# Kernel optimization log

Hardware: AMD Instinct MI355X
Metric: run time of the kernel (lower is better)

The kernel has to match this reference:

```python
import jax, jax.numpy as jnp
import numpy as np


def setup_inputs() -> dict:
    key = jax.random.key(0)
    k1, k2, k3 = jax.random.split(key, 3)
    N, C, V, T, K = 32, 64, 25, 1024, 3
    x = jax.random.normal(k1, (N, C, V, T), dtype=jnp.float32)
    # grouped 1x1 conv weight: per node v, maps C -> K*C. torch weight (C*K*V, C, 1, 1)
    W = jax.random.normal(k2, (V, K * C, C), dtype=jnp.float32) * 0.05
    # adjacency buffer A[k, w, v] (src node w -> dst node v, partition k)
    A = jax.random.uniform(k3, (K, V, V), dtype=jnp.float32)
    return {"x": x, "W": W, "A": A}


def reference(x, W, A):
    # x: [N, C, V, T]; W: [V, K*C, C]; A: [K, V, V]
    N, C, V, T = x.shape
    K = A.shape[0]
    # permute(0,2,1,3): [N, V, C, T]; grouped 1x1 conv == per-node matmul C -> K*C
    y = jnp.einsum('ncvt,voc->nvot', x, W)          # [N, V, K*C, T]
    # view (N, V, C*K, T) with output-channel layout o = c*K + k -> split to (C, K)
    y = y.reshape(N, V, C, K, T)                     # [N, V(src=w), C, K, T]
    # einsum('kwv,nckwt->ncvt')
    out = jnp.einsum('kwv,nwckt->ncvt', A, y)        # [N, C, V, T]
    return out
```

## Files before the change

### kernel.cpp

```cpp
#include <hip/hip_runtime.h>

#define Nn 32
#define Cc 64
#define Vv 25
#define Tt 1024

typedef __attribute__((ext_vector_type(4))) float f32x4;
typedef __attribute__((ext_vector_type(8))) short bf16x8;
typedef __attribute__((ext_vector_type(4))) unsigned short u16x4;

__device__ __forceinline__ unsigned short f2bf(float f) {
    union { float f; unsigned u; } a; a.f = f;
    unsigned u = a.u;
    u += 0x7fff + ((u >> 16) & 1);
    return (unsigned short)(u >> 16);
}

__device__ __forceinline__ void gl_lds16(const unsigned short* g, unsigned short* l) {
    __builtin_amdgcn_global_load_lds(
        (const __attribute__((address_space(1))) unsigned int*)g,
        (__attribute__((address_space(3))) unsigned int*)l, 16, 0, 0);
}


__global__ __launch_bounds__(256) void prep_fused(
        const float* __restrict__ x, const float* __restrict__ W,
        const float* __restrict__ A, unsigned short* __restrict__ xb,
        unsigned short* __restrict__ Weff) {
    int bid = blockIdx.x;
    if (bid < Vv * Vv) {
        int v = bid / Vv;
        int w = bid - v * Vv;
        float a0 = A[(0 * Vv + w) * Vv + v];
        float a1 = A[(1 * Vv + w) * Vv + v];
        float a2 = A[(2 * Vv + w) * Vv + v];
        const float* Wb = W + (size_t)w * 192 * 64;
        unsigned short* o = Weff + (size_t)(v * Vv + w) * 4096;
        int c  = threadIdx.x >> 2;
        int c0 = (threadIdx.x & 3) * 16;
        #pragma unroll
        for (int i = 0; i < 16; ++i) {
            int cp = c0 + i;
            float val = a0 * Wb[(c * 3 + 0) * 64 + cp]
                      + a1 * Wb[(c * 3 + 1) * 64 + cp]
                      + a2 * Wb[(c * 3 + 2) * 64 + cp];
            int jl = cp >> 3;
            o[c * 64 + ((jl ^ (c & 7)) << 3) + (cp & 7)] = f2bf(val);
        }
        return;
    }
    int pid = bid - Vv * Vv;
    int n = pid / (Vv * 8);
    int rem = pid - n * (Vv * 8);
    int w = rem >> 3;
    int t0 = (rem & 7) << 7;

    int tid = threadIdx.x;
    int wv = tid >> 6;
    int l  = tid & 63;
    int jl = l & 7;
    int tg = l >> 3;

    int tbase = t0 + wv * 32 + tg * 4;
    const float* xn = x + ((size_t)(n * Cc) * Vv + w) * Tt + tbase;
    unsigned short* dst = xb + ((size_t)(n * Vv + w) * Tt) * 64;

    f32x4 f[8];
    #pragma unroll
    for (int k = 0; k < 8; ++k) {
        int r = jl * 8 + k;
        f[k] = __builtin_nontemporal_load(
            (const f32x4*)(xn + (size_t)r * (Vv * Tt)));
    }
    #pragma unroll
    for (int j = 0; j < 4; ++j) {
        bf16x8 o;
        #pragma unroll
        for (int k = 0; k < 8; ++k) o[k] = (short)f2bf(f[k][j]);
        int tl = tbase + j;
        int pc = jl ^ (tl & 7);
        *(bf16x8*)&dst[(size_t)tl * 64 + pc * 8] = o;
    }
}

__global__ __launch_bounds__(256, 2) void gc_fast(
        const unsigned short* __restrict__ xb,
        const unsigned short* __restrict__ Weff,
        float* __restrict__ out) {
    __shared__ __align__(16) unsigned short wa[8][4096];

    int bid = blockIdx.x;
    int xcd = bid & 7;
    int lid = bid >> 3;
    int v = lid % Vv;
    int s = lid / Vv;
    int slice = (xcd << 4) + s;
    int n  = slice >> 2;
    int t0 = (slice & 3) << 8;

    int tid = threadIdx.x;
    int lane = tid & 63, wv = tid >> 6;
    int m = lane & 15, quad = lane >> 4;

    const unsigned short* wg = Weff + (size_t)v * (Vv * 4096);
    const unsigned short* xbase = xb + ((size_t)(n * Vv) * Tt + t0) * 64;

    int coff0 = ((quad)     ^ (m & 7)) << 3;
    int coff1 = ((4 + quad) ^ (m & 7)) << 3;
    int trow[4], arow[4];
    #pragma unroll
    for (int ni = 0; ni < 4; ++ni) trow[ni] = (wv * 64 + ni * 16 + m) * 64;
    #pragma unroll
    for (int mi = 0; mi < 4; ++mi) arow[mi] = (mi * 16 + m) * 64;

    f32x4 acc[4][4];
    #pragma unroll
    for (int i = 0; i < 4; ++i)
        #pragma unroll
        for (int j = 0; j < 4; ++j)
            acc[i][j] = (f32x4){0.f, 0.f, 0.f, 0.f};

    bf16x8 b0v[8], b1v[8], b2v[8];

#define SB __builtin_amdgcn_sched_barrier(0)
#define VMCNT(N_) asm volatile("s_waitcnt vmcnt(" #N_ ")" ::: "memory")

#define ISSUE_A(WBUF, w_) do { \
    const unsigned short* s_ = wg + (size_t)(w_) * 4096 + tid * 8; \
    gl_lds16(s_,        &wa[WBUF][tid * 8]); \
    gl_lds16(s_ + 2048, &wa[WBUF][2048 + tid * 8]); \
} while (0)

#define ISSUE_B(BN, w_) do { \
    const unsigned short* xw_ = xbase + (size_t)(w_) * (Tt * 64); \
    _Pragma("unroll") \
    for (int ni_ = 0; ni_ < 4; ++ni_) { \
        BN[ni_]     = *(const bf16x8*)(xw_ + trow[ni_] + coff0); \
        BN[ni_ + 4] = *(const bf16x8*)(xw_ + trow[ni_] + coff1); \
    } \
} while (0)

#define COMP(RBUF, BC) do { \
    const unsigned short* cur_ = &wa[RBUF][0]; \
    bf16x8 af_[8]; \
    _Pragma("unroll") \
    for (int mi_ = 0; mi_ < 4; ++mi_) { \
        af_[mi_]     = *(const bf16x8*)(cur_ + arow[mi_] + coff0); \
        af_[mi_ + 4] = *(const bf16x8*)(cur_ + arow[mi_] + coff1); \
    } \
    __builtin_amdgcn_s_setprio(1); \
    _Pragma("unroll") \
    for (int mi_ = 0; mi_ < 4; ++mi_) \
        _Pragma("unroll") \
        for (int ni_ = 0; ni_ < 4; ++ni_) \
            acc[mi_][ni_] = __builtin_amdgcn_mfma_f32_16x16x32_bf16( \
                af_[mi_], BC[ni_], acc[mi_][ni_], 0, 0, 0); \
    _Pragma("unroll") \
    for (int mi_ = 0; mi_ < 4; ++mi_) \
        _Pragma("unroll") \
        for (int ni_ = 0; ni_ < 4; ++ni_) \
            acc[mi_][ni_] = __builtin_amdgcn_mfma_f32_16x16x32_bf16( \
                af_[mi_ + 4], BC[ni_ + 4], acc[mi_][ni_], 0, 0, 0); \
    __builtin_amdgcn_s_setprio(0); \
} while (0)

#define DSTEP(R0, R1, W4, W5, C0, C1, I2, I3, w_, N3, N6) do { \
    ISSUE_B(I2, (w_) + 2); \
    ISSUE_A(W4, (w_) + 4); \
    ISSUE_A(W5, (w_) + 5); \
    SB; VMCNT(N3); SB; \
    __builtin_amdgcn_s_barrier(); \
    SB; \
    COMP(R0, C0); \
    SB; \
    ISSUE_B(I3, (w_) + 3); \
    SB; VMCNT(N6); SB; \
    COMP(R1, C1); \
    SB; \
} while (0)

    ISSUE_B(b0v, 0);
    ISSUE_B(b1v, 1);
    ISSUE_A(0, 0);
    ISSUE_A(1, 1);
    ISSUE_A(2, 2);
    ISSUE_A(3, 3);
    SB;

    DSTEP(0, 1, 4, 5, b0v, b1v, b2v, b0v,  0, 16, 20);
    DSTEP(2, 3, 6, 7, b2v, b0v, b1v, b2v,  2, 24, 20);
    DSTEP(4, 5, 0, 1, b1v, b2v, b0v, b1v,  4, 24, 20);
    DSTEP(6, 7, 2, 3, b0v, b1v, b2v, b0v,  6, 24, 20);
    DSTEP(0, 1, 4, 5, b2v, b0v, b1v, b2v,  8, 24, 20);
    DSTEP(2, 3, 6, 7, b1v, b2v, b0v, b1v, 10, 24, 20);
    DSTEP(4, 5, 0, 1, b0v, b1v, b2v, b0v, 12, 24, 20);
    DSTEP(6, 7, 2, 3, b2v, b0v, b1v, b2v, 14, 24, 20);
    DSTEP(0, 1, 4, 5, b1v, b2v, b0v, b1v, 16, 24, 20);
    DSTEP(2, 3, 6, 7, b0v, b1v, b2v, b0v, 18, 24, 20);

    ISSUE_B(b1v, 22);
    ISSUE_A(0, 24);
    SB; VMCNT(22); SB;
    __builtin_amdgcn_s_barrier();
    SB;
    COMP(4, b2v);
    SB;
    ISSUE_B(b2v, 23);
    SB; VMCNT(18); SB;
    COMP(5, b0v);
    SB;

    ISSUE_B(b0v, 24);
    SB; VMCNT(18); SB;
    __builtin_amdgcn_s_barrier();
    SB;
    COMP(6, b1v);
    SB; VMCNT(10); SB;
    COMP(7, b2v);
    SB;

    VMCNT(0);
    SB;
    __builtin_amdgcn_s_barrier();
    SB;
    COMP(0, b0v);

#undef DSTEP
#undef COMP
#undef ISSUE_B
#undef ISSUE_A
#undef VMCNT
#undef SB

    float* og = out + ((size_t)n * Cc * Vv + v) * Tt + t0 + wv * 64 + m;
    #pragma unroll
    for (int mi = 0; mi < 4; ++mi)
        #pragma unroll
        for (int r = 0; r < 4; ++r) {
            int c = mi * 16 + quad * 4 + r;
            float* orow = og + (size_t)c * Vv * Tt;
            #pragma unroll
            for (int ni = 0; ni < 4; ++ni)
                __builtin_nontemporal_store(acc[mi][ni][r], &orow[ni * 16]);
        }
}


__global__ __launch_bounds__(256) void weff_prep_plain(
        const float* __restrict__ W, const float* __restrict__ A,
        unsigned short* __restrict__ Weff) {
    int v = blockIdx.x / Vv;
    int w = blockIdx.x - v * Vv;
    float a0 = A[(0 * Vv + w) * Vv + v];
    float a1 = A[(1 * Vv + w) * Vv + v];
    float a2 = A[(2 * Vv + w) * Vv + v];
    const float* Wb = W + (size_t)w * 192 * 64;
    unsigned short* o = Weff + (size_t)(v * Vv + w) * 4096;
    int e0 = threadIdx.x * 16;
    #pragma unroll
    for (int i = 0; i < 16; ++i) {
        int e = e0 + i;
        int c = e >> 6, cp = e & 63;
        float val = a0 * Wb[(c * 3 + 0) * 64 + cp]
                  + a1 * Wb[(c * 3 + 1) * 64 + cp]
                  + a2 * Wb[(c * 3 + 2) * 64 + cp];
        o[e] = f2bf(val);
    }
}

__global__ __launch_bounds__(256, 2) void gc_plain(
        const float* __restrict__ x, const unsigned short* __restrict__ Weff,
        float* __restrict__ out) {
    __shared__ __align__(16) unsigned short xs[256 * 72];
    __shared__ __align__(16) unsigned short wa[64 * 72];
    int bid = blockIdx.x;
    int xcd = bid & 7;
    int lid = bid >> 3;
    int v, s;
    if (lid < 13 * 16) { v = lid % 13;            s = lid / 13; }
    else { int l2 = lid - 13 * 16; v = 13 + l2 % 12; s = l2 / 12; }
    int slice = (xcd << 4) + s;
    int n  = slice >> 2;
    int t0 = (slice & 3) << 8;
    int tid  = threadIdx.x;
    int lane = tid & 63;
    int wv   = tid >> 6;
    int m    = lane & 15;
    int quad = lane >> 4;
    int cc = tid & 7;
    int tt = tid >> 3;
    f32x4 acc[4][4];
    #pragma unroll
    for (int i = 0; i < 4; ++i)
        #pragma unroll
        for (int j = 0; j < 4; ++j)
            acc[i][j] = (f32x4){0.f, 0.f, 0.f, 0.f};
    const float* xg = x + (size_t)n * Cc * Vv * Tt + t0 + tt * 4;
    const bf16x8* wg = (const bf16x8*)(Weff + (size_t)v * Vv * 4096);
    for (int w = 0; w < Vv; ++w) {
        if (w) __syncthreads();
        #pragma unroll
        for (int r = 0; r < 2; ++r) {
            int q = r * 256 + tid;
            int c = q >> 3, b = q & 7;
            *(bf16x8*)&wa[c * 72 + b * 8] = wg[w * 512 + q];
        }
        {
            bf16x8 rows[8];
            #pragma unroll
            for (int i = 0; i < 8; ++i) {
                int cp = cc * 8 + i;
                const float* p = xg + ((size_t)cp * Vv + w) * Tt;
                float4 f0 = *(const float4*)p;
                float4 f1 = *(const float4*)(p + 128);
                rows[0][i] = (short)f2bf(f0.x); rows[1][i] = (short)f2bf(f0.y);
                rows[2][i] = (short)f2bf(f0.z); rows[3][i] = (short)f2bf(f0.w);
                rows[4][i] = (short)f2bf(f1.x); rows[5][i] = (short)f2bf(f1.y);
                rows[6][i] = (short)f2bf(f1.z); rows[7][i] = (short)f2bf(f1.w);
            }
            #pragma unroll
            for (int j = 0; j < 4; ++j) {
                *(bf16x8*)&xs[(tt * 4 + j) * 72 + cc * 8]       = rows[j];
                *(bf16x8*)&xs[(128 + tt * 4 + j) * 72 + cc * 8] = rows[4 + j];
            }
        }
        __syncthreads();
        #pragma unroll
        for (int kc = 0; kc < 2; ++kc) {
            int ko = kc * 32 + quad * 8;
            bf16x8 afr[4], bfr[4];
            #pragma unroll
            for (int mi = 0; mi < 4; ++mi)
                afr[mi] = *(const bf16x8*)&wa[(mi * 16 + m) * 72 + ko];
            #pragma unroll
            for (int ni = 0; ni < 4; ++ni)
                bfr[ni] = *(const bf16x8*)&xs[(wv * 64 + ni * 16 + m) * 72 + ko];
            #pragma unroll
            for (int mi = 0; mi < 4; ++mi)
                #pragma unroll
                for (int ni = 0; ni < 4; ++ni)
                    acc[mi][ni] = __builtin_amdgcn_mfma_f32_16x16x32_bf16(
                        afr[mi], bfr[ni], acc[mi][ni], 0, 0, 0);
        }
    }
    float* og = out + ((size_t)n * Cc * Vv + v) * Tt + t0 + wv * 64 + m;
    #pragma unroll
    for (int mi = 0; mi < 4; ++mi)
        #pragma unroll
        for (int r = 0; r < 4; ++r) {
            int c = mi * 16 + quad * 4 + r;
            float* orow = og + (size_t)c * Vv * Tt;
            #pragma unroll
            for (int ni = 0; ni < 4; ++ni)
                orow[ni * 16] = acc[mi][ni][r];
        }
}

extern "C" void kernel_launch(void* const* d_in, const int* in_sizes, int n_in,
                              void* d_out, int out_size, void* d_ws, size_t ws_size,
                              hipStream_t stream) {
    const float* x = (const float*)d_in[0];
    const float* W = (const float*)d_in[1];
    const float* A = (const float*)d_in[2];
    float* out = (float*)d_out;

    const size_t xb_elems   = (size_t)Nn * Vv * Tt * 64;
    const size_t weff_elems = (size_t)Vv * Vv * 4096;
    const size_t need = (xb_elems + weff_elems) * sizeof(unsigned short);

    if (ws_size >= need) {
        unsigned short* xb   = (unsigned short*)d_ws;
        unsigned short* Weff = xb + xb_elems;
        prep_fused<<<dim3(Vv * Vv + Nn * Vv * 8), dim3(256), 0, stream>>>(x, W, A, xb, Weff);
        gc_fast<<<dim3(3200), dim3(256), 0, stream>>>(xb, Weff, out);
    } else {
        unsigned short* Weff = (unsigned short*)d_ws;
        weff_prep_plain<<<dim3(Vv * Vv), dim3(256), 0, stream>>>(W, A, Weff);
        gc_plain<<<dim3(3200), dim3(256), 0, stream>>>(x, Weff, out);
    }
}
```

Baseline: 501.5 us.

## Store bf16 x in MFMA fragment order for fully coalesced B loads

The prep kernel now writes the bf16 copy of x pre-arranged in the exact per-lane fragment order the MFMA B operand uses. The main kernel can then load each B fragment with one contiguous 16-byte read per lane instead of swizzled row-strided reads. The prep kernel changes its block decomposition to 4 time slices per (n,w) and gathers with scalar strided nontemporal loads, which may make the x read less efficient.

```diff
diff --git a/kernel.cpp b/kernel.cpp
--- a/kernel.cpp
+++ b/kernel.cpp
@@ -50,36 +50,38 @@
         return;
     }
     int pid = bid - Vv * Vv;
-    int n = pid / (Vv * 8);
-    int rem = pid - n * (Vv * 8);
-    int w = rem >> 3;
-    int t0 = (rem & 7) << 7;
+    int n = pid / (Vv * 4);
+    int rem = pid - n * (Vv * 4);
+    int w = rem >> 2;
+    int sl = rem & 3;
 
     int tid = threadIdx.x;
-    int wv = tid >> 6;
+    int wq = tid >> 6;
     int l  = tid & 63;
-    int jl = l & 7;
-    int tg = l >> 3;
-
-    int tbase = t0 + wv * 32 + tg * 4;
-    const float* xn = x + ((size_t)(n * Cc) * Vv + w) * Tt + tbase;
-    unsigned short* dst = xb + ((size_t)(n * Vv + w) * Tt) * 64;
-
-    f32x4 f[8];
-    #pragma unroll
-    for (int k = 0; k < 8; ++k) {
-        int r = jl * 8 + k;
-        f[k] = __builtin_nontemporal_load(
-            (const f32x4*)(xn + (size_t)r * (Vv * Tt)));
-    }
-    #pragma unroll
-    for (int j = 0; j < 4; ++j) {
-        bf16x8 o;
-        #pragma unroll
-        for (int k = 0; k < 8; ++k) o[k] = (short)f2bf(f[k][j]);
-        int tl = tbase + j;
-        int pc = jl ^ (tl & 7);
-        *(bf16x8*)&dst[(size_t)tl * 64 + pc * 8] = o;
+    int quad = l >> 4, m = l & 15;
+
+    const float* xw = x + ((size_t)n * Cc * Vv + w) * Tt + sl * 256 + wq * 64 + m;
+    unsigned short* dst = xb +
+        ((((size_t)(n * Vv + w) * 4 + sl) * 2048) + (size_t)wq * 512 + l) * 8;
+
+    #pragma unroll
+    for (int kc = 0; kc < 2; ++kc) {
+        float vals[4][8];
+        #pragma unroll
+        for (int kk = 0; kk < 8; ++kk) {
+            int cp = (kc * 4 + quad) * 8 + kk;
+            const float* row = xw + (size_t)cp * (Vv * Tt);
+            #pragma unroll
+            for (int ni = 0; ni < 4; ++ni)
+                vals[ni][kk] = __builtin_nontemporal_load(row + ni * 16);
+        }
+        #pragma unroll
+        for (int ni = 0; ni < 4; ++ni) {
+            bf16x8 o;
+            #pragma unroll
+            for (int kk = 0; kk < 8; ++kk) o[kk] = (short)f2bf(vals[ni][kk]);
+            *(bf16x8*)&dst[(size_t)(kc * 256 + ni * 64) * 8] = o;
+        }
     }
 }
 
@@ -96,22 +98,24 @@
     int s = lid / Vv;
     int slice = (xcd << 4) + s;
     int n  = slice >> 2;
-    int t0 = (slice & 3) << 8;
+    int sl = slice & 3;
+    int t0 = sl << 8;
 
     int tid = threadIdx.x;
     int lane = tid & 63, wv = tid >> 6;
     int m = lane & 15, quad = lane >> 4;
 
     const unsigned short* wg = Weff + (size_t)v * (Vv * 4096);
-    const unsigned short* xbase = xb + ((size_t)(n * Vv) * Tt + t0) * 64;
+    const unsigned short* xbase = xb + ((size_t)(n * Vv * 4 + sl)) * 2048 * 8;
 
     int coff0 = ((quad)     ^ (m & 7)) << 3;
     int coff1 = ((4 + quad) ^ (m & 7)) << 3;
-    int trow[4], arow[4];
-    #pragma unroll
-    for (int ni = 0; ni < 4; ++ni) trow[ni] = (wv * 64 + ni * 16 + m) * 64;
+    int arow[4];
     #pragma unroll
     for (int mi = 0; mi < 4; ++mi) arow[mi] = (mi * 16 + m) * 64;
+    int boff[8];
+    #pragma unroll
+    for (int q = 0; q < 8; ++q) boff[q] = ((wv * 8 + q) * 64 + lane) * 8;
 
     f32x4 acc[4][4];
     #pragma unroll
@@ -132,12 +136,10 @@
 } while (0)
 
 #define ISSUE_B(BN, w_) do { \
-    const unsigned short* xw_ = xbase + (size_t)(w_) * (Tt * 64); \
+    const unsigned short* xw_ = xbase + (size_t)(w_) * 65536; \
     _Pragma("unroll") \
-    for (int ni_ = 0; ni_ < 4; ++ni_) { \
-        BN[ni_]     = *(const bf16x8*)(xw_ + trow[ni_] + coff0); \
-        BN[ni_ + 4] = *(const bf16x8*)(xw_ + trow[ni_] + coff1); \
-    } \
+    for (int q_ = 0; q_ < 8; ++q_) \
+        BN[q_] = *(const bf16x8*)(xw_ + boff[q_]); \
 } while (0)
 
 #define COMP(RBUF, BC) do { \
@@ -371,7 +373,7 @@
     if (ws_size >= need) {
         unsigned short* xb   = (unsigned short*)d_ws;
         unsigned short* Weff = xb + xb_elems;
-        prep_fused<<<dim3(Vv * Vv + Nn * Vv * 8), dim3(256), 0, stream>>>(x, W, A, xb, Weff);
+        prep_fused<<<dim3(Vv * Vv + Nn * Vv * 4), dim3(256), 0, stream>>>(x, W, A, xb, Weff);
         gc_fast<<<dim3(3200), dim3(256), 0, stream>>>(xb, Weff, out);
     } else {
         unsigned short* Weff = (unsigned short*)d_ws;
```

Measured after the change: 503.1 us. No clear change (+0.3%).
